# Optimization experiments

Hardware: AMD Instinct MI355X
Metric: run time of the kernel (lower is better)

## Reference

```python
import jax, jax.numpy as jnp
import numpy as np

N, F_NODE, F_FLOW, H, E, B, L = 131072, 64, 16, 128, 2097152, 256, 32


def setup_inputs() -> dict:
    key = jax.random.key(0)
    ks = jax.random.split(key, 24)
    gn = lambda k, s, sc: jax.random.normal(k, s, jnp.float32) * sc
    s_in = 1.0 / np.sqrt(F_NODE)
    s_h = 1.0 / np.sqrt(H)
    s_f = 1.0 / np.sqrt(F_FLOW)
    s_c = 1.0 / np.sqrt(2 * H + H // 2)
    inp = {
        "x": gn(ks[0], (N, F_NODE), 1.0),
        "edge_index": jax.random.randint(ks[1], (2, E), 0, N),
        "batch": jnp.sort(jax.random.randint(ks[2], (N,), 0, B)),
        "path_idx": jax.random.randint(ks[3], (B, L), 0, N),
        "path_len": jax.random.randint(ks[4], (B,), 1, L + 1),
        "flow": gn(ks[5], (B, F_FLOW), 1.0),
        # SAGEConv1: out = mean_agg(x_j) @ Wl.T + b + x_i @ Wr.T
        "Wl1": gn(ks[6], (H, F_NODE), s_in), "Wr1": gn(ks[7], (H, F_NODE), s_in), "b1": gn(ks[8], (H,), s_in),
        "Wl2": gn(ks[9], (H, H), s_h), "Wr2": gn(ks[10], (H, H), s_h), "b2": gn(ks[11], (H,), s_h),
        # LSTM (torch gate order i,f,g,o)
        "Wih": gn(ks[12], (4 * H, H), s_h), "Whh": gn(ks[13], (4 * H, H), s_h),
        "bih": gn(ks[14], (4 * H,), s_h), "bhh": gn(ks[15], (4 * H,), s_h),
        # flow encoder Linear(F_FLOW, H//2)
        "Wf": gn(ks[16], (H // 2, F_FLOW), s_f), "bf": gn(ks[17], (H // 2,), s_f),
        # scorer MLP: Linear(2H+H//2, H) -> ReLU -> Linear(H, 1)
        "Ws1": gn(ks[18], (H, 2 * H + H // 2), s_c), "bs1": gn(ks[19], (H,), s_c),
        "Ws2": gn(ks[20], (1, H), s_h), "bs2": gn(ks[21], (1,), s_h),
    }
    return inp


def _sage(x, src, dst, Wl, Wr, b, n):
    agg = jax.ops.segment_sum(x[src], dst, num_segments=n)  # [n, d]
    cnt = jax.ops.segment_sum(jnp.ones((src.shape[0],), x.dtype), dst, num_segments=n)
    mean = agg / jnp.maximum(cnt, 1.0)[:, None]
    return mean @ Wl.T + b + x @ Wr.T


def _lstm_final_h(seq, valid, Wih, Whh, bih, bhh):
    # seq: [B, L, H], valid: [B, L] bool; returns h at each path's last valid step
    b, l, h = seq.shape
    h0 = jnp.zeros((b, h), seq.dtype)

    def step(carry, inp):
        hp, cp = carry
        x_t, v = inp  # [B,H], [B]
        gates = x_t @ Wih.T + hp @ Whh.T + bih + bhh
        i, f, g, o = jnp.split(gates, 4, axis=-1)
        c_new = jax.nn.sigmoid(f) * cp + jax.nn.sigmoid(i) * jnp.tanh(g)
        h_new = jax.nn.sigmoid(o) * jnp.tanh(c_new)
        m = v[:, None]
        return (jnp.where(m, h_new, hp), jnp.where(m, c_new, cp)), None

    (hf, _), _ = jax.lax.scan(step, (h0, h0),
                              (jnp.swapaxes(seq, 0, 1), jnp.swapaxes(valid, 0, 1)))
    return hf


def reference(x, edge_index, batch, path_idx, path_len, flow,
              Wl1, Wr1, b1, Wl2, Wr2, b2,
              Wih, Whh, bih, bhh, Wf, bf, Ws1, bs1, Ws2, bs2):
    n = x.shape[0]
    src, dst = edge_index[0], edge_index[1]
    h1 = jax.nn.relu(_sage(x, src, dst, Wl1, Wr1, b1, n))
    node_emb = jax.nn.relu(_sage(h1, src, dst, Wl2, Wr2, b2, n))

    # global mean pool per graph
    gsum = jax.ops.segment_sum(node_emb, batch, num_segments=B)
    gcnt = jax.ops.segment_sum(jnp.ones((n,), node_emb.dtype), batch, num_segments=B)
    graph_emb = gsum / jnp.maximum(gcnt, 1.0)[:, None]  # [B, H]

    flow_emb = jax.nn.relu(flow @ Wf.T + bf)  # [B, H//2]

    path_seq = node_emb[path_idx]  # [B, L, H]
    valid = jnp.arange(L)[None, :] < path_len[:, None]  # [B, L]
    path_emb = _lstm_final_h(path_seq, valid, Wih, Whh, bih, bhh)  # [B, H]

    combined = jnp.concatenate([graph_emb, path_emb, flow_emb], axis=-1)
    hidden = jax.nn.relu(combined @ Ws1.T + bs1)
    scores = hidden @ Ws2.T + bs2  # [B, 1]
    return scores[:, 0]  # matches torch.cat of per-path [1] outputs -> [B]
```

## Files before the change

kernel.cpp:

```cpp
#include <hip/hip_runtime.h>
#include <hip/hip_bf16.h>

#define N_NODES 131072
#define N_EDGES 2097152
#define BATCHES 256
#define LPATH   32
#define NB   256
#define NPB  512
#define GB   256
#define EPB  8192

typedef __hip_bfloat16 bf16;
using short8  = __attribute__((ext_vector_type(8))) short;
using floatx4 = __attribute__((ext_vector_type(4))) float;
using floatx2 = __attribute__((ext_vector_type(2))) float;

__device__ __forceinline__ float bl(unsigned u){ union {unsigned x; float f;} c; c.x = u << 16; return c.f; }
__device__ __forceinline__ float bh(unsigned u){ union {unsigned x; float f;} c; c.x = u & 0xffff0000u; return c.f; }
__device__ __forceinline__ unsigned packbf(float lo, float hi){
  bf16 l = __float2bfloat16(lo), h = __float2bfloat16(hi);
  unsigned short lu, hu;
  __builtin_memcpy(&lu, &l, 2); __builtin_memcpy(&hu, &h, 2);
  return (unsigned)lu | ((unsigned)hu << 16);
}
__device__ __forceinline__ float frcp(float x){ return __builtin_amdgcn_rcpf(x); }
__device__ __forceinline__ float sigf(float x){ return frcp(1.f + __expf(-x)); }
__device__ __forceinline__ float tanh_fast(float x){ return fmaf(2.f, frcp(1.f + __expf(-2.f * x)), -1.f); }

__global__ void prep_k(const float* __restrict__ Wl1, const float* __restrict__ Wr1,
                       const float* __restrict__ Wl2, const float* __restrict__ Wr2,
                       const float* __restrict__ Wih, const float* __restrict__ Whh,
                       const float* __restrict__ bih, const float* __restrict__ bhh,
                       bf16* __restrict__ Wcat1, bf16* __restrict__ Wcat2,
                       bf16* __restrict__ WihB, bf16* __restrict__ WhhB, float* __restrict__ bsumF){
  int g = blockIdx.x * 256 + threadIdx.x;
  if (g < 16384) {
    int h = g >> 7, k = g & 127;
    float v = (k < 64) ? Wl1[h * 64 + k] : Wr1[h * 64 + (k - 64)];
    Wcat1[g] = __float2bfloat16(v);
  } else if (g < 49152) {
    int q = g - 16384;
    int h = q >> 8, k = q & 255;
    float v = (k < 128) ? Wl2[h * 128 + k] : Wr2[h * 128 + (k - 128)];
    Wcat2[q] = __float2bfloat16(v);
  } else if (g < 114688) {
    int q = g - 49152;
    WihB[q] = __float2bfloat16(Wih[q]);
  } else if (g < 180224) {
    int q = g - 114688;
    WhhB[q] = __float2bfloat16(Whh[q]);
  } else if (g < 180736) {
    int k = g - 180224;
    bsumF[k] = bih[k] + bhh[k];
  }
}

__global__ void xb8_k(const float* __restrict__ x, unsigned* __restrict__ xb8, bf16* __restrict__ Acat1){
  int g = blockIdx.x * 256 + threadIdx.x;
  int n = g >> 4, p = g & 15;
  float4 v = *(const float4*)(x + (size_t)n * 64 + p * 4);
  uint2 wb; wb.x = packbf(v.x, v.y); wb.y = packbf(v.z, v.w);
  *(uint2*)(Acat1 + (size_t)n * 128 + 64 + p * 4) = wb;
  int w = 0;
  w = __builtin_amdgcn_cvt_pk_fp8_f32(v.x, v.y, w, false);
  w = __builtin_amdgcn_cvt_pk_fp8_f32(v.z, v.w, w, true);
  xb8[(size_t)n * 16 + p] = (unsigned)w;
}

__global__ void bounds_k(const int* __restrict__ batch, int* __restrict__ starts){
  int b = threadIdx.x;
  int lo = 0, hi = N_NODES;
  while (lo < hi){ int mid = (lo + hi) >> 1; if (batch[mid] < b) lo = mid + 1; else hi = mid; }
  starts[b] = lo;
  if (b == 0) starts[BATCHES] = N_NODES;
}

__global__ void cntA_k(const int* __restrict__ dst, int* __restrict__ cntA){
  __shared__ int h[NB];
  int tid = threadIdx.x;
  h[tid] = 0;
  __syncthreads();
  int base = blockIdx.x * EPB;
  #pragma unroll
  for (int i = 0; i < EPB / 256; ++i){
    int d = dst[base + i * 256 + tid];
    atomicAdd(&h[d >> 9], 1);
  }
  __syncthreads();
  cntA[tid * GB + blockIdx.x] = h[tid];
}

__global__ void scan1_k(const int* __restrict__ cnt, int* __restrict__ ofsA, int* __restrict__ bsum){
  __shared__ int sh[256];
  int t = threadIdx.x, i = blockIdx.x * 256 + t;
  int v = cnt[i];
  sh[t] = v; __syncthreads();
  int inc = v;
  for (int d = 1; d < 256; d <<= 1){
    int add = (t >= d) ? sh[t - d] : 0;
    __syncthreads();
    inc += add; sh[t] = inc;
    __syncthreads();
  }
  ofsA[i] = inc - v;
  if (t == 255) bsum[blockIdx.x] = inc;
}

__global__ void scan2_k(const int* __restrict__ bsum, int* __restrict__ bsumEx){
  __shared__ int sh[NB];
  int t = threadIdx.x;
  int v = bsum[t];
  sh[t] = v; __syncthreads();
  int inc = v;
  for (int d = 1; d < NB; d <<= 1){
    int add = (t >= d) ? sh[t - d] : 0;
    __syncthreads();
    inc += add; sh[t] = inc;
    __syncthreads();
  }
  bsumEx[t] = inc - v;
}

__global__ void passA2_k(const int* __restrict__ src, const int* __restrict__ dst,
                         const int* __restrict__ ofsA, const int* __restrict__ bsumEx,
                         unsigned* __restrict__ ebuf){
  __shared__ int cur[NB];
  int tid = threadIdx.x;
  cur[tid] = ofsA[tid * GB + blockIdx.x] + bsumEx[tid];
  __syncthreads();
  int base = blockIdx.x * EPB;
  #pragma unroll
  for (int i = 0; i < EPB / 256; ++i){
    int e = base + i * 256 + tid;
    int s = src[e], d = dst[e];
    int p = atomicAdd(&cur[d >> 9], 1);
    ebuf[p] = (unsigned)s | ((unsigned)(d & (NPB - 1)) << 17);
  }
}

__global__ void passB_k(const unsigned* __restrict__ ebuf, const int* __restrict__ bsumEx,
                        int* __restrict__ offs, int* __restrict__ srcS){
  __shared__ int ncnt[NPB];
  __shared__ int pairs[256];
  __shared__ int nofs[NPB];
  int k = blockIdx.x, tid = threadIdx.x;
  int bs = bsumEx[k];
  int be = (k < NB - 1) ? bsumEx[k + 1] : N_EDGES;
  ncnt[tid] = 0; ncnt[tid + 256] = 0;
  __syncthreads();
  for (int i = bs + tid; i < be; i += 256)
    atomicAdd(&ncnt[ebuf[i] >> 17], 1);
  __syncthreads();
  int p = ncnt[2 * tid] + ncnt[2 * tid + 1];
  pairs[tid] = p;
  __syncthreads();
  int inc = p;
  for (int d = 1; d < 256; d <<= 1){
    int add = (tid >= d) ? pairs[tid - d] : 0;
    __syncthreads();
    inc += add; pairs[tid] = inc;
    __syncthreads();
  }
  int ex = inc - p;
  nofs[2 * tid]     = ex;
  nofs[2 * tid + 1] = ex + ncnt[2 * tid];
  __syncthreads();
  offs[k * NPB + tid]       = bs + nofs[tid];
  offs[k * NPB + tid + 256] = bs + nofs[tid + 256];
  if (k == NB - 1 && tid == 0) offs[N_NODES] = N_EDGES;
  ncnt[tid] = nofs[tid]; ncnt[tid + 256] = nofs[tid + 256];
  __syncthreads();
  for (int i = bs + tid; i < be; i += 256){
    unsigned w = ebuf[i];
    int loc = w >> 17, sv = w & 0x1FFFF;
    int pp = atomicAdd(&ncnt[loc], 1);
    srcS[bs + pp] = sv;
  }
}

__global__ void agg1_k(const unsigned* __restrict__ xb8, const int* __restrict__ offs,
                       const int* __restrict__ srcS, bf16* __restrict__ Acat1){
  int wid = threadIdx.x >> 6, lane = threadIdx.x & 63;
  int n = blockIdx.x * 4 + wid;
  int s = offs[n], e = offs[n + 1];
  int slot = lane >> 3, fl = lane & 7;
  floatx2 a0={0,0}, a1={0,0}, a2={0,0}, a3={0,0};
  floatx2 c0={0,0}, c1={0,0}, c2={0,0}, c3={0,0};
  int i = s + slot;
  for (; i + 8 < e; i += 16){
    int sv0 = srcS[i], sv1 = srcS[i + 8];
    uint2 u = *(const uint2*)(xb8 + (size_t)sv0 * 16 + fl * 2);
    uint2 v = *(const uint2*)(xb8 + (size_t)sv1 * 16 + fl * 2);
    a0 += __builtin_amdgcn_cvt_pk_f32_fp8(u.x, false);
    a1 += __builtin_amdgcn_cvt_pk_f32_fp8(u.x, true);
    a2 += __builtin_amdgcn_cvt_pk_f32_fp8(u.y, false);
    a3 += __builtin_amdgcn_cvt_pk_f32_fp8(u.y, true);
    c0 += __builtin_amdgcn_cvt_pk_f32_fp8(v.x, false);
    c1 += __builtin_amdgcn_cvt_pk_f32_fp8(v.x, true);
    c2 += __builtin_amdgcn_cvt_pk_f32_fp8(v.y, false);
    c3 += __builtin_amdgcn_cvt_pk_f32_fp8(v.y, true);
  }
  if (i < e){
    int sv0 = srcS[i];
    uint2 u = *(const uint2*)(xb8 + (size_t)sv0 * 16 + fl * 2);
    a0 += __builtin_amdgcn_cvt_pk_f32_fp8(u.x, false);
    a1 += __builtin_amdgcn_cvt_pk_f32_fp8(u.x, true);
    a2 += __builtin_amdgcn_cvt_pk_f32_fp8(u.y, false);
    a3 += __builtin_amdgcn_cvt_pk_f32_fp8(u.y, true);
  }
  a0 += c0; a1 += c1; a2 += c2; a3 += c3;
  float f[8] = {a0.x, a0.y, a1.x, a1.y, a2.x, a2.y, a3.x, a3.y};
  #pragma unroll
  for (int j = 0; j < 8; ++j){
    f[j] += __shfl_xor(f[j], 8);
    f[j] += __shfl_xor(f[j], 16);
    f[j] += __shfl_xor(f[j], 32);
  }
  if (slot == 0){
    int d = e - s; if (d < 1) d = 1;
    float inv = 1.f / (float)d;
    uint4 w;
    w.x = packbf(f[0] * inv, f[1] * inv);
    w.y = packbf(f[2] * inv, f[3] * inv);
    w.z = packbf(f[4] * inv, f[5] * inv);
    w.w = packbf(f[6] * inv, f[7] * inv);
    *(uint4*)(Acat1 + (size_t)n * 128 + fl * 8) = w;
  }
}

__global__ void cvt8_k(const bf16* __restrict__ Acat2, unsigned* __restrict__ h1f8){
  int g = blockIdx.x * 256 + threadIdx.x;
  int n = g >> 5, p = g & 31;
  uint2 u = *(const uint2*)(Acat2 + (size_t)n * 256 + 128 + p * 4);
  int w = 0;
  w = __builtin_amdgcn_cvt_pk_fp8_f32(bl(u.x), bh(u.x), w, false);
  w = __builtin_amdgcn_cvt_pk_fp8_f32(bl(u.y), bh(u.y), w, true);
  h1f8[(size_t)n * 32 + p] = (unsigned)w;
}

__global__ void agg2_k(const int* __restrict__ offs, const int* __restrict__ srcS,
                       const unsigned* __restrict__ h1f8, bf16* __restrict__ Acat2){
  int wid = threadIdx.x >> 6, lane = threadIdx.x & 63;
  int n = blockIdx.x * 4 + wid;
  int s = offs[n], e = offs[n + 1];
  int slot = lane >> 4, fl = lane & 15;
  floatx2 a0={0,0}, a1={0,0}, a2={0,0}, a3={0,0};
  floatx2 c0={0,0}, c1={0,0}, c2={0,0}, c3={0,0};
  int i = s + slot;
  for (; i + 4 < e; i += 8){
    int sv0 = srcS[i], sv1 = srcS[i + 4];
    uint2 u = *(const uint2*)(h1f8 + (size_t)sv0 * 32 + fl * 2);
    uint2 v = *(const uint2*)(h1f8 + (size_t)sv1 * 32 + fl * 2);
    a0 += __builtin_amdgcn_cvt_pk_f32_fp8(u.x, false);
    a1 += __builtin_amdgcn_cvt_pk_f32_fp8(u.x, true);
    a2 += __builtin_amdgcn_cvt_pk_f32_fp8(u.y, false);
    a3 += __builtin_amdgcn_cvt_pk_f32_fp8(u.y, true);
    c0 += __builtin_amdgcn_cvt_pk_f32_fp8(v.x, false);
    c1 += __builtin_amdgcn_cvt_pk_f32_fp8(v.x, true);
    c2 += __builtin_amdgcn_cvt_pk_f32_fp8(v.y, false);
    c3 += __builtin_amdgcn_cvt_pk_f32_fp8(v.y, true);
  }
  if (i < e){
    int sv0 = srcS[i];
    uint2 u = *(const uint2*)(h1f8 + (size_t)sv0 * 32 + fl * 2);
    a0 += __builtin_amdgcn_cvt_pk_f32_fp8(u.x, false);
    a1 += __builtin_amdgcn_cvt_pk_f32_fp8(u.x, true);
    a2 += __builtin_amdgcn_cvt_pk_f32_fp8(u.y, false);
    a3 += __builtin_amdgcn_cvt_pk_f32_fp8(u.y, true);
  }
  a0 += c0; a1 += c1; a2 += c2; a3 += c3;
  float f[8] = {a0.x, a0.y, a1.x, a1.y, a2.x, a2.y, a3.x, a3.y};
  #pragma unroll
  for (int j = 0; j < 8; ++j){
    f[j] += __shfl_xor(f[j], 16);
    f[j] += __shfl_xor(f[j], 32);
  }
  if (slot == 0){
    int d = e - s; if (d < 1) d = 1;
    float inv = 1.f / (float)d;
    uint4 w;
    w.x = packbf(f[0] * inv, f[1] * inv);
    w.y = packbf(f[2] * inv, f[3] * inv);
    w.z = packbf(f[4] * inv, f[5] * inv);
    w.w = packbf(f[6] * inv, f[7] * inv);
    *(uint4*)(Acat2 + (size_t)n * 256 + fl * 8) = w;
  }
}

__global__ __launch_bounds__(256) void gemm_k(const bf16* __restrict__ A, int lda,
                                              const bf16* __restrict__ W, int K,
                                              const float* __restrict__ bias,
                                              void* __restrict__ out, int ldo, int outF32, int relu,
                                              const int* __restrict__ ridx){
  __shared__ bf16 Wl[128][136];
  int tid = threadIdx.x;
  int wid = tid >> 6, lane = tid & 63;
  int l16 = lane & 15, quad = lane >> 4;
  int rowBase  = blockIdx.x * 64 + wid * 16;
  int colGroup = blockIdx.y * 128;
  int arow = rowBase + l16;
  if (ridx) arow = ridx[arow];
  floatx4 acc[8] = {};
  int nStage = K >> 7;
  for (int ks = 0; ks < nStage; ++ks){
    __syncthreads();
    for (int c = tid; c < 2048; c += 256){
      int r = c >> 4, kc = (c & 15) << 3;
      *(uint4*)(&Wl[r][kc]) = *(const uint4*)(W + (size_t)(colGroup + r) * K + ks * 128 + kc);
    }
    __syncthreads();
    for (int kk = 0; kk < 4; ++kk){
      short8 af = *(const short8*)(A + (size_t)arow * lda + ks * 128 + kk * 32 + quad * 8);
      #pragma unroll
      for (int c = 0; c < 8; ++c){
        short8 bq = *(const short8*)(&Wl[c * 16 + l16][kk * 32 + quad * 8]);
        acc[c] = __builtin_amdgcn_mfma_f32_16x16x32_bf16(af, bq, acc[c], 0, 0, 0);
      }
    }
  }
  #pragma unroll
  for (int c = 0; c < 8; ++c){
    int col = colGroup + c * 16 + l16;
    float bv = bias ? bias[col] : 0.f;
    #pragma unroll
    for (int r = 0; r < 4; ++r){
      int row = rowBase + quad * 4 + r;
      float v = acc[c][r] + bv;
      if (relu) v = fmaxf(v, 0.f);
      if (outF32) ((float*)out)[(size_t)row * ldo + col] = v;
      else        ((bf16*)out)[(size_t)row * ldo + col]  = __float2bfloat16(v);
    }
  }
}

__global__ void pool_k(const bf16* __restrict__ ne, const int* __restrict__ starts, float* __restrict__ comb){
  __shared__ float sh[8][128];
  int b = blockIdx.x;
  int q = threadIdx.x >> 6, lane = threadIdx.x & 63;
  int s = starts[b], e = starts[b + 1];
  float a0 = 0.f, a1 = 0.f;
  for (int i = s + q; i < e; i += 8){
    unsigned u = *(const unsigned*)(ne + (size_t)i * 128 + lane * 2);
    a0 += bl(u); a1 += bh(u);
  }
  sh[q][lane * 2] = a0; sh[q][lane * 2 + 1] = a1;
  __syncthreads();
  if (threadIdx.x < 128){
    int f = threadIdx.x;
    float tot = 0.f;
    #pragma unroll
    for (int k = 0; k < 8; ++k) tot += sh[k][f];
    int d = e - s; if (d < 1) d = 1;
    comb[b * 320 + f] = tot / (float)d;
  }
}

__global__ void flow_k(const float* __restrict__ flow, const float* __restrict__ Wf,
                       const float* __restrict__ bfv, float* __restrict__ comb){
  int g = blockIdx.x * 256 + threadIdx.x;
  int b = g >> 6, j = g & 63;
  float acc = bfv[j];
  for (int k = 0; k < 16; ++k)
    acc += flow[b * 16 + k] * Wf[j * 16 + k];
  comb[b * 320 + 256 + j] = fmaxf(acc, 0.f);
}

__global__ __launch_bounds__(256, 1) void lstm_k(const bf16* __restrict__ Whh, const float* __restrict__ pre,
                                                 const int* __restrict__ path_len, float* __restrict__ comb){
  __shared__ bf16 hbuf[2][16][136];
  int tid = threadIdx.x;
  int w = tid >> 6, lane = tid & 63;
  int l16 = lane & 15, quad = lane >> 4;
  int b0 = blockIdx.x * 16;

  short8 wb[4][2][4];
  #pragma unroll
  for (int q = 0; q < 4; ++q)
    #pragma unroll
    for (int hf = 0; hf < 2; ++hf){
      const bf16* rp = Whh + (size_t)(q * 128 + w * 32 + hf * 16 + l16) * 128 + quad * 8;
      #pragma unroll
      for (int ks = 0; ks < 4; ++ks) wb[q][hf][ks] = *(const short8*)(rp + ks * 32);
    }

  int lenr[4];
  #pragma unroll
  for (int r = 0; r < 4; ++r){
    int L = path_len[b0 + quad * 4 + r];
    if (L < 1) L = 1; if (L > LPATH) L = LPATH;
    lenr[r] = L;
  }
  int maxlen = 1;
  for (int i = 0; i < 16; ++i){
    int L = path_len[b0 + i];
    if (L > LPATH) L = LPATH;
    if (L > maxlen) maxlen = L;
  }

  for (int i = tid; i < 1088; i += 256) ((unsigned*)&hbuf[0][0][0])[i] = 0;

  const float* pb[4];
  #pragma unroll
  for (int r = 0; r < 4; ++r)
    pb[r] = pre + (size_t)(b0 + quad * 4 + r) * LPATH * 512 + w * 32 + l16;

  float pv[4][2][4];
  #pragma unroll
  for (int q = 0; q < 4; ++q)
    #pragma unroll
    for (int hf = 0; hf < 2; ++hf)
      #pragma unroll
      for (int r = 0; r < 4; ++r)
        pv[q][hf][r] = pb[r][q * 128 + hf * 16];

  float cst[2][4] = {}, hst[2][4] = {};

  for (int t = 0; t < maxlen; ++t){
    int cur = t & 1, nxt = cur ^ 1;
    __syncthreads();
    short8 af[4];
    #pragma unroll
    for (int ks = 0; ks < 4; ++ks)
      af[ks] = *(const short8*)(&hbuf[cur][l16][ks * 32 + quad * 8]);
    int tn = (t + 1 < maxlen) ? t + 1 : t;
    float pnext[4][2][4];
    #pragma unroll
    for (int q = 0; q < 4; ++q)
      #pragma unroll
      for (int hf = 0; hf < 2; ++hf)
        #pragma unroll
        for (int r = 0; r < 4; ++r)
          pnext[q][hf][r] = pb[r][tn * 512 + q * 128 + hf * 16];
    floatx4 acc[4][2];
    #pragma unroll
    for (int q = 0; q < 4; ++q)
      #pragma unroll
      for (int hf = 0; hf < 2; ++hf){
        acc[q][hf][0] = pv[q][hf][0]; acc[q][hf][1] = pv[q][hf][1];
        acc[q][hf][2] = pv[q][hf][2]; acc[q][hf][3] = pv[q][hf][3];
      }
    #pragma unroll
    for (int ks = 0; ks < 4; ++ks)
      #pragma unroll
      for (int q = 0; q < 4; ++q)
        #pragma unroll
        for (int hf = 0; hf < 2; ++hf)
          acc[q][hf] = __builtin_amdgcn_mfma_f32_16x16x32_bf16(af[ks], wb[q][hf][ks], acc[q][hf], 0, 0, 0);
    #pragma unroll
    for (int hf = 0; hf < 2; ++hf)
      #pragma unroll
      for (int r = 0; r < 4; ++r){
        float ig = sigf(acc[0][hf][r]);
        float fg = sigf(acc[1][hf][r]);
        float gg = tanh_fast(acc[2][hf][r]);
        float og = sigf(acc[3][hf][r]);
        float cn = fmaf(fg, cst[hf][r], ig * gg);
        float hn = og * tanh_fast(cn);
        bool vld = t < lenr[r];
        cst[hf][r] = vld ? cn : cst[hf][r];
        hst[hf][r] = vld ? hn : hst[hf][r];
        hbuf[nxt][quad * 4 + r][w * 32 + hf * 16 + l16] = __float2bfloat16(hst[hf][r]);
      }
    #pragma unroll
    for (int q = 0; q < 4; ++q)
      #pragma unroll
      for (int hf = 0; hf < 2; ++hf)
        #pragma unroll
        for (int r = 0; r < 4; ++r)
          pv[q][hf][r] = pnext[q][hf][r];
  }

  #pragma unroll
  for (int hf = 0; hf < 2; ++hf)
    #pragma unroll
    for (int r = 0; r < 4; ++r)
      comb[(b0 + quad * 4 + r) * 320 + 128 + w * 32 + hf * 16 + l16] = hst[hf][r];
}

__global__ void head_k(const float* __restrict__ comb, const float* __restrict__ Ws1, const float* __restrict__ bs1,
                       const float* __restrict__ Ws2, const float* __restrict__ bs2, float* __restrict__ out){
  __shared__ float cl[320];
  __shared__ float red[128];
  int b = blockIdx.x, j = threadIdx.x;
  for (int k = j; k < 320; k += 128) cl[k] = comb[b * 320 + k];
  __syncthreads();
  float acc = bs1[j];
  const float4* wr = (const float4*)(Ws1 + (size_t)j * 320);
  #pragma unroll 4
  for (int kc = 0; kc < 80; ++kc){
    float4 u = wr[kc];
    int k = kc * 4;
    acc += u.x * cl[k] + u.y * cl[k + 1] + u.z * cl[k + 2] + u.w * cl[k + 3];
  }
  float hv = fmaxf(acc, 0.f);
  red[j] = hv * Ws2[j];
  __syncthreads();
  for (int s = 64; s > 0; s >>= 1){ if (j < s) red[j] += red[j + s]; __syncthreads(); }
  if (j == 0) out[b] = red[0] + bs2[0];
}

constexpr size_t OFF_OFFS   = 0;
constexpr size_t OFF_CNTA   = 524544;
constexpr size_t OFF_OFSA   = OFF_CNTA   + 262144;
constexpr size_t OFF_BSUM   = OFF_OFSA   + 262144;
constexpr size_t OFF_BSUMEX = OFF_BSUM   + 1024;
constexpr size_t OFF_STARTS = OFF_BSUMEX + 1024;
constexpr size_t OFF_SRCS   = OFF_STARTS + 2048;
constexpr size_t OFF_WCAT1  = OFF_SRCS   + 8388608;
constexpr size_t OFF_WCAT2  = OFF_WCAT1  + 32768;
constexpr size_t OFF_WIHB   = OFF_WCAT2  + 65536;
constexpr size_t OFF_WHHB   = OFF_WIHB   + 131072;
constexpr size_t OFF_BSUMF  = OFF_WHHB   + 131072;
constexpr size_t OFF_COMB   = OFF_BSUMF  + 2048;
constexpr size_t OFF_ACAT1  = OFF_COMB   + 327680;
constexpr size_t OFF_ACAT2  = OFF_ACAT1  + 33554432;
constexpr size_t OFF_H1F8   = OFF_ACAT1;
constexpr size_t OFF_EBUF   = OFF_ACAT2;
constexpr size_t OFF_PRE    = OFF_ACAT2  + 2097152;
constexpr size_t OFF_XB8    = OFF_ACAT2  + 50331648;

extern "C" void kernel_launch(void* const* d_in, const int* in_sizes, int n_in,
                              void* d_out, int out_size, void* d_ws, size_t ws_size,
                              hipStream_t stream){
  const float* x      = (const float*)d_in[0];
  const int* edge     = (const int*)d_in[1];
  const int* batch    = (const int*)d_in[2];
  const int* path_idx = (const int*)d_in[3];
  const int* path_len = (const int*)d_in[4];
  const float* flow   = (const float*)d_in[5];
  const float* Wl1 = (const float*)d_in[6];
  const float* Wr1 = (const float*)d_in[7];
  const float* b1  = (const float*)d_in[8];
  const float* Wl2 = (const float*)d_in[9];
  const float* Wr2 = (const float*)d_in[10];
  const float* b2  = (const float*)d_in[11];
  const float* Wih = (const float*)d_in[12];
  const float* Whh = (const float*)d_in[13];
  const float* bih = (const float*)d_in[14];
  const float* bhh = (const float*)d_in[15];
  const float* Wf  = (const float*)d_in[16];
  const float* bfv = (const float*)d_in[17];
  const float* Ws1 = (const float*)d_in[18];
  const float* bs1 = (const float*)d_in[19];
  const float* Ws2 = (const float*)d_in[20];
  const float* bs2 = (const float*)d_in[21];

  char* ws = (char*)d_ws;
  int* offs    = (int*)(ws + OFF_OFFS);
  int* cntA    = (int*)(ws + OFF_CNTA);
  int* ofsA    = (int*)(ws + OFF_OFSA);
  int* bsum    = (int*)(ws + OFF_BSUM);
  int* bsumEx  = (int*)(ws + OFF_BSUMEX);
  int* starts  = (int*)(ws + OFF_STARTS);
  int* srcS    = (int*)(ws + OFF_SRCS);
  bf16* Wcat1  = (bf16*)(ws + OFF_WCAT1);
  bf16* Wcat2  = (bf16*)(ws + OFF_WCAT2);
  bf16* WihB   = (bf16*)(ws + OFF_WIHB);
  bf16* WhhB   = (bf16*)(ws + OFF_WHHB);
  float* bsumF = (float*)(ws + OFF_BSUMF);
  float* comb  = (float*)(ws + OFF_COMB);
  bf16* Acat1  = (bf16*)(ws + OFF_ACAT1);
  bf16* node_emb = Acat1;
  bf16* Acat2  = (bf16*)(ws + OFF_ACAT2);
  unsigned* h1f8 = (unsigned*)(ws + OFF_H1F8);
  unsigned* ebuf = (unsigned*)(ws + OFF_EBUF);
  float* pre   = (float*)(ws + OFF_PRE);
  unsigned* xb8 = (unsigned*)(ws + OFF_XB8);

  prep_k<<<707, 256, 0, stream>>>(Wl1, Wr1, Wl2, Wr2, Wih, Whh, bih, bhh, Wcat1, Wcat2, WihB, WhhB, bsumF);
  xb8_k<<<N_NODES / 16, 256, 0, stream>>>(x, xb8, Acat1);
  bounds_k<<<1, 256, 0, stream>>>(batch, starts);
  cntA_k<<<GB, 256, 0, stream>>>(edge + N_EDGES, cntA);
  scan1_k<<<NB, 256, 0, stream>>>(cntA, ofsA, bsum);
  scan2_k<<<1, NB, 0, stream>>>(bsum, bsumEx);
  passA2_k<<<GB, 256, 0, stream>>>(edge, edge + N_EDGES, ofsA, bsumEx, ebuf);
  passB_k<<<NB, 256, 0, stream>>>(ebuf, bsumEx, offs, srcS);
  agg1_k<<<N_NODES / 4, 256, 0, stream>>>(xb8, offs, srcS, Acat1);
  gemm_k<<<dim3(N_NODES / 64, 1), 256, 0, stream>>>(Acat1, 128, Wcat1, 128, b1, Acat2 + 128, 256, 0, 1, nullptr);
  cvt8_k<<<N_NODES / 8, 256, 0, stream>>>(Acat2, h1f8);
  agg2_k<<<N_NODES / 4, 256, 0, stream>>>(offs, srcS, h1f8, Acat2);
  gemm_k<<<dim3(N_NODES / 64, 1), 256, 0, stream>>>(Acat2, 256, Wcat2, 256, b2, node_emb, 128, 0, 1, nullptr);
  pool_k<<<BATCHES, 512, 0, stream>>>(node_emb, starts, comb);
  flow_k<<<64, 256, 0, stream>>>(flow, Wf, bfv, comb);
  gemm_k<<<dim3(BATCHES * LPATH / 64, 4), 256, 0, stream>>>(node_emb, 128, WihB, 128, bsumF, pre, 512, 1, 0, path_idx);
  lstm_k<<<BATCHES / 16, 256, 0, stream>>>(WhhB, pre, path_len, comb);
  head_k<<<BATCHES, 128, 0, stream>>>(comb, Ws1, bs1, Ws2, bs2, (float*)d_out);
}
```

Baseline: 444.6 us.

## Merge small prep kernels into fused launches and unroll agg2 gather loop

```diff
diff --git a/kernel.cpp b/kernel.cpp
--- a/kernel.cpp
+++ b/kernel.cpp
@@ -27,67 +27,67 @@
 __device__ __forceinline__ float sigf(float x){ return frcp(1.f + __expf(-x)); }
 __device__ __forceinline__ float tanh_fast(float x){ return fmaf(2.f, frcp(1.f + __expf(-2.f * x)), -1.f); }
 
-__global__ void prep_k(const float* __restrict__ Wl1, const float* __restrict__ Wr1,
-                       const float* __restrict__ Wl2, const float* __restrict__ Wr2,
-                       const float* __restrict__ Wih, const float* __restrict__ Whh,
-                       const float* __restrict__ bih, const float* __restrict__ bhh,
-                       bf16* __restrict__ Wcat1, bf16* __restrict__ Wcat2,
-                       bf16* __restrict__ WihB, bf16* __restrict__ WhhB, float* __restrict__ bsumF){
-  int g = blockIdx.x * 256 + threadIdx.x;
-  if (g < 16384) {
-    int h = g >> 7, k = g & 127;
-    float v = (k < 64) ? Wl1[h * 64 + k] : Wr1[h * 64 + (k - 64)];
-    Wcat1[g] = __float2bfloat16(v);
-  } else if (g < 49152) {
-    int q = g - 16384;
-    int h = q >> 8, k = q & 255;
-    float v = (k < 128) ? Wl2[h * 128 + k] : Wr2[h * 128 + (k - 128)];
-    Wcat2[q] = __float2bfloat16(v);
-  } else if (g < 114688) {
-    int q = g - 49152;
-    WihB[q] = __float2bfloat16(Wih[q]);
-  } else if (g < 180224) {
-    int q = g - 114688;
-    WhhB[q] = __float2bfloat16(Whh[q]);
-  } else if (g < 180736) {
-    int k = g - 180224;
-    bsumF[k] = bih[k] + bhh[k];
-  }
-}
-
-__global__ void xb8_k(const float* __restrict__ x, unsigned* __restrict__ xb8, bf16* __restrict__ Acat1){
-  int g = blockIdx.x * 256 + threadIdx.x;
-  int n = g >> 4, p = g & 15;
-  float4 v = *(const float4*)(x + (size_t)n * 64 + p * 4);
-  uint2 wb; wb.x = packbf(v.x, v.y); wb.y = packbf(v.z, v.w);
-  *(uint2*)(Acat1 + (size_t)n * 128 + 64 + p * 4) = wb;
-  int w = 0;
-  w = __builtin_amdgcn_cvt_pk_fp8_f32(v.x, v.y, w, false);
-  w = __builtin_amdgcn_cvt_pk_fp8_f32(v.z, v.w, w, true);
-  xb8[(size_t)n * 16 + p] = (unsigned)w;
-}
-
-__global__ void bounds_k(const int* __restrict__ batch, int* __restrict__ starts){
-  int b = threadIdx.x;
-  int lo = 0, hi = N_NODES;
-  while (lo < hi){ int mid = (lo + hi) >> 1; if (batch[mid] < b) lo = mid + 1; else hi = mid; }
-  starts[b] = lo;
-  if (b == 0) starts[BATCHES] = N_NODES;
-}
-
-__global__ void cntA_k(const int* __restrict__ dst, int* __restrict__ cntA){
+__global__ void mega0_k(const float* __restrict__ x, unsigned* __restrict__ xb8, bf16* __restrict__ Acat1,
+                        const int* __restrict__ dst, int* __restrict__ cntA,
+                        const float* __restrict__ Wl1, const float* __restrict__ Wr1,
+                        const float* __restrict__ Wl2, const float* __restrict__ Wr2,
+                        const float* __restrict__ Wih, const float* __restrict__ Whh,
+                        const float* __restrict__ bih, const float* __restrict__ bhh,
+                        bf16* __restrict__ Wcat1, bf16* __restrict__ Wcat2,
+                        bf16* __restrict__ WihB, bf16* __restrict__ WhhB, float* __restrict__ bsumF,
+                        const int* __restrict__ batch, int* __restrict__ starts){
   __shared__ int h[NB];
-  int tid = threadIdx.x;
-  h[tid] = 0;
-  __syncthreads();
-  int base = blockIdx.x * EPB;
-  #pragma unroll
-  for (int i = 0; i < EPB / 256; ++i){
-    int d = dst[base + i * 256 + tid];
-    atomicAdd(&h[d >> 9], 1);
-  }
-  __syncthreads();
-  cntA[tid * GB + blockIdx.x] = h[tid];
+  int bid = blockIdx.x, tid = threadIdx.x;
+  if (bid < 8192){
+    int g = bid * 256 + tid;
+    int n = g >> 4, p = g & 15;
+    float4 v = *(const float4*)(x + (size_t)n * 64 + p * 4);
+    uint2 wb; wb.x = packbf(v.x, v.y); wb.y = packbf(v.z, v.w);
+    *(uint2*)(Acat1 + (size_t)n * 128 + 64 + p * 4) = wb;
+    int w = 0;
+    w = __builtin_amdgcn_cvt_pk_fp8_f32(v.x, v.y, w, false);
+    w = __builtin_amdgcn_cvt_pk_fp8_f32(v.z, v.w, w, true);
+    xb8[(size_t)n * 16 + p] = (unsigned)w;
+  } else if (bid < 8448){
+    int cb = bid - 8192;
+    h[tid] = 0;
+    __syncthreads();
+    int base = cb * EPB;
+    #pragma unroll
+    for (int i = 0; i < EPB / 256; ++i){
+      int d = dst[base + i * 256 + tid];
+      atomicAdd(&h[d >> 9], 1);
+    }
+    __syncthreads();
+    cntA[tid * GB + cb] = h[tid];
+  } else if (bid < 9155){
+    int g = (bid - 8448) * 256 + tid;
+    if (g < 16384) {
+      int hh = g >> 7, k = g & 127;
+      float v = (k < 64) ? Wl1[hh * 64 + k] : Wr1[hh * 64 + (k - 64)];
+      Wcat1[g] = __float2bfloat16(v);
+    } else if (g < 49152) {
+      int q = g - 16384;
+      int hh = q >> 8, k = q & 255;
+      float v = (k < 128) ? Wl2[hh * 128 + k] : Wr2[hh * 128 + (k - 128)];
+      Wcat2[q] = __float2bfloat16(v);
+    } else if (g < 114688) {
+      int q = g - 49152;
+      WihB[q] = __float2bfloat16(Wih[q]);
+    } else if (g < 180224) {
+      int q = g - 114688;
+      WhhB[q] = __float2bfloat16(Whh[q]);
+    } else if (g < 180736) {
+      int k = g - 180224;
+      bsumF[k] = bih[k] + bhh[k];
+    }
+  } else {
+    int b = tid;
+    int lo = 0, hi = N_NODES;
+    while (lo < hi){ int mid = (lo + hi) >> 1; if (batch[mid] < b) lo = mid + 1; else hi = mid; }
+    starts[b] = lo;
+    if (b == 0) starts[BATCHES] = N_NODES;
+  }
 }
 
 __global__ void scan1_k(const int* __restrict__ cnt, int* __restrict__ ofsA, int* __restrict__ bsum){
@@ -106,27 +106,22 @@
   if (t == 255) bsum[blockIdx.x] = inc;
 }
 
-__global__ void scan2_k(const int* __restrict__ bsum, int* __restrict__ bsumEx){
-  __shared__ int sh[NB];
-  int t = threadIdx.x;
-  int v = bsum[t];
-  sh[t] = v; __syncthreads();
+__global__ void passA2_k(const int* __restrict__ src, const int* __restrict__ dst,
+                         const int* __restrict__ ofsA, const int* __restrict__ bsum,
+                         unsigned* __restrict__ ebuf){
+  __shared__ int cur[NB];
+  __shared__ int sc[NB];
+  int tid = threadIdx.x;
+  int v = bsum[tid];
+  sc[tid] = v; __syncthreads();
   int inc = v;
   for (int d = 1; d < NB; d <<= 1){
-    int add = (t >= d) ? sh[t - d] : 0;
-    __syncthreads();
-    inc += add; sh[t] = inc;
-    __syncthreads();
-  }
-  bsumEx[t] = inc - v;
-}
-
-__global__ void passA2_k(const int* __restrict__ src, const int* __restrict__ dst,
-                         const int* __restrict__ ofsA, const int* __restrict__ bsumEx,
-                         unsigned* __restrict__ ebuf){
-  __shared__ int cur[NB];
-  int tid = threadIdx.x;
-  cur[tid] = ofsA[tid * GB + blockIdx.x] + bsumEx[tid];
+    int add = (tid >= d) ? sc[tid - d] : 0;
+    __syncthreads();
+    inc += add; sc[tid] = inc;
+    __syncthreads();
+  }
+  cur[tid] = ofsA[tid * GB + blockIdx.x] + (inc - v);
   __syncthreads();
   int base = blockIdx.x * EPB;
   #pragma unroll
@@ -138,14 +133,26 @@
   }
 }
 
-__global__ void passB_k(const unsigned* __restrict__ ebuf, const int* __restrict__ bsumEx,
+__global__ void passB_k(const unsigned* __restrict__ ebuf, const int* __restrict__ bsum,
                         int* __restrict__ offs, int* __restrict__ srcS){
   __shared__ int ncnt[NPB];
   __shared__ int pairs[256];
   __shared__ int nofs[NPB];
+  __shared__ int sc[NB];
   int k = blockIdx.x, tid = threadIdx.x;
-  int bs = bsumEx[k];
-  int be = (k < NB - 1) ? bsumEx[k + 1] : N_EDGES;
+  int v = bsum[tid];
+  sc[tid] = v; __syncthreads();
+  int inc0 = v;
+  for (int d = 1; d < NB; d <<= 1){
+    int add = (tid >= d) ? sc[tid - d] : 0;
+    __syncthreads();
+    inc0 += add; sc[tid] = inc0;
+    __syncthreads();
+  }
+  sc[tid] = inc0 - v;
+  __syncthreads();
+  int bs = sc[k];
+  int be = (k < NB - 1) ? sc[k + 1] : N_EDGES;
   ncnt[tid] = 0; ncnt[tid + 256] = 0;
   __syncthreads();
   for (int i = bs + tid; i < be; i += 256)
@@ -245,22 +252,34 @@
   int s = offs[n], e = offs[n + 1];
   int slot = lane >> 4, fl = lane & 15;
   floatx2 a0={0,0}, a1={0,0}, a2={0,0}, a3={0,0};
+  floatx2 b0={0,0}, b1={0,0}, b2={0,0}, b3={0,0};
   floatx2 c0={0,0}, c1={0,0}, c2={0,0}, c3={0,0};
+  floatx2 d0={0,0}, d1={0,0}, d2={0,0}, d3={0,0};
   int i = s + slot;
-  for (; i + 4 < e; i += 8){
-    int sv0 = srcS[i], sv1 = srcS[i + 4];
+  for (; i + 12 < e; i += 16){
+    int sv0 = srcS[i], sv1 = srcS[i + 4], sv2 = srcS[i + 8], sv3 = srcS[i + 12];
     uint2 u = *(const uint2*)(h1f8 + (size_t)sv0 * 32 + fl * 2);
     uint2 v = *(const uint2*)(h1f8 + (size_t)sv1 * 32 + fl * 2);
+    uint2 w = *(const uint2*)(h1f8 + (size_t)sv2 * 32 + fl * 2);
+    uint2 z = *(const uint2*)(h1f8 + (size_t)sv3 * 32 + fl * 2);
     a0 += __builtin_amdgcn_cvt_pk_f32_fp8(u.x, false);
     a1 += __builtin_amdgcn_cvt_pk_f32_fp8(u.x, true);
     a2 += __builtin_amdgcn_cvt_pk_f32_fp8(u.y, false);
     a3 += __builtin_amdgcn_cvt_pk_f32_fp8(u.y, true);
-    c0 += __builtin_amdgcn_cvt_pk_f32_fp8(v.x, false);
-    c1 += __builtin_amdgcn_cvt_pk_f32_fp8(v.x, true);
-    c2 += __builtin_amdgcn_cvt_pk_f32_fp8(v.y, false);
-    c3 += __builtin_amdgcn_cvt_pk_f32_fp8(v.y, true);
-  }
-  if (i < e){
+    b0 += __builtin_amdgcn_cvt_pk_f32_fp8(v.x, false);
+    b1 += __builtin_amdgcn_cvt_pk_f32_fp8(v.x, true);
+    b2 += __builtin_amdgcn_cvt_pk_f32_fp8(v.y, false);
+    b3 += __builtin_amdgcn_cvt_pk_f32_fp8(v.y, true);
+    c0 += __builtin_amdgcn_cvt_pk_f32_fp8(w.x, false);
+    c1 += __builtin_amdgcn_cvt_pk_f32_fp8(w.x, true);
+    c2 += __builtin_amdgcn_cvt_pk_f32_fp8(w.y, false);
+    c3 += __builtin_amdgcn_cvt_pk_f32_fp8(w.y, true);
+    d0 += __builtin_amdgcn_cvt_pk_f32_fp8(z.x, false);
+    d1 += __builtin_amdgcn_cvt_pk_f32_fp8(z.x, true);
+    d2 += __builtin_amdgcn_cvt_pk_f32_fp8(z.y, false);
+    d3 += __builtin_amdgcn_cvt_pk_f32_fp8(z.y, true);
+  }
+  for (; i < e; i += 4){
     int sv0 = srcS[i];
     uint2 u = *(const uint2*)(h1f8 + (size_t)sv0 * 32 + fl * 2);
     a0 += __builtin_amdgcn_cvt_pk_f32_fp8(u.x, false);
@@ -268,6 +287,8 @@
     a2 += __builtin_amdgcn_cvt_pk_f32_fp8(u.y, false);
     a3 += __builtin_amdgcn_cvt_pk_f32_fp8(u.y, true);
   }
+  a0 += b0; a1 += b1; a2 += b2; a3 += b3;
+  c0 += d0; c1 += d1; c2 += d2; c3 += d3;
   a0 += c0; a1 += c1; a2 += c2; a3 += c3;
   float f[8] = {a0.x, a0.y, a1.x, a1.y, a2.x, a2.y, a3.x, a3.y};
   #pragma unroll
@@ -333,36 +354,38 @@
   }
 }
 
-__global__ void pool_k(const bf16* __restrict__ ne, const int* __restrict__ starts, float* __restrict__ comb){
+__global__ void poolflow_k(const bf16* __restrict__ ne, const int* __restrict__ starts,
+                           const float* __restrict__ flow, const float* __restrict__ Wf,
+                           const float* __restrict__ bfv, float* __restrict__ comb){
   __shared__ float sh[8][128];
-  int b = blockIdx.x;
-  int q = threadIdx.x >> 6, lane = threadIdx.x & 63;
-  int s = starts[b], e = starts[b + 1];
-  float a0 = 0.f, a1 = 0.f;
-  for (int i = s + q; i < e; i += 8){
-    unsigned u = *(const unsigned*)(ne + (size_t)i * 128 + lane * 2);
-    a0 += bl(u); a1 += bh(u);
-  }
-  sh[q][lane * 2] = a0; sh[q][lane * 2 + 1] = a1;
-  __syncthreads();
-  if (threadIdx.x < 128){
-    int f = threadIdx.x;
-    float tot = 0.f;
-    #pragma unroll
-    for (int k = 0; k < 8; ++k) tot += sh[k][f];
-    int d = e - s; if (d < 1) d = 1;
-    comb[b * 320 + f] = tot / (float)d;
-  }
-}
-
-__global__ void flow_k(const float* __restrict__ flow, const float* __restrict__ Wf,
-                       const float* __restrict__ bfv, float* __restrict__ comb){
-  int g = blockIdx.x * 256 + threadIdx.x;
-  int b = g >> 6, j = g & 63;
-  float acc = bfv[j];
-  for (int k = 0; k < 16; ++k)
-    acc += flow[b * 16 + k] * Wf[j * 16 + k];
-  comb[b * 320 + 256 + j] = fmaxf(acc, 0.f);
+  int bid = blockIdx.x;
+  if (bid < 256){
+    int b = bid;
+    int q = threadIdx.x >> 6, lane = threadIdx.x & 63;
+    int s = starts[b], e = starts[b + 1];
+    float a0 = 0.f, a1 = 0.f;
+    for (int i = s + q; i < e; i += 8){
+      unsigned u = *(const unsigned*)(ne + (size_t)i * 128 + lane * 2);
+      a0 += bl(u); a1 += bh(u);
+    }
+    sh[q][lane * 2] = a0; sh[q][lane * 2 + 1] = a1;
+    __syncthreads();
+    if (threadIdx.x < 128){
+      int f = threadIdx.x;
+      float tot = 0.f;
+      #pragma unroll
+      for (int k = 0; k < 8; ++k) tot += sh[k][f];
+      int d = e - s; if (d < 1) d = 1;
+      comb[b * 320 + f] = tot / (float)d;
+    }
+  } else {
+    int g = (bid - 256) * 512 + threadIdx.x;
+    int b = g >> 6, j = g & 63;
+    float acc = bfv[j];
+    for (int k = 0; k < 16; ++k)
+      acc += flow[b * 16 + k] * Wf[j * 16 + k];
+    comb[b * 320 + 256 + j] = fmaxf(acc, 0.f);
+  }
 }
 
 __global__ __launch_bounds__(256, 1) void lstm_k(const bf16* __restrict__ Whh, const float* __restrict__ pre,
@@ -503,8 +526,7 @@
 constexpr size_t OFF_CNTA   = 524544;
 constexpr size_t OFF_OFSA   = OFF_CNTA   + 262144;
 constexpr size_t OFF_BSUM   = OFF_OFSA   + 262144;
-constexpr size_t OFF_BSUMEX = OFF_BSUM   + 1024;
-constexpr size_t OFF_STARTS = OFF_BSUMEX + 1024;
+constexpr size_t OFF_STARTS = OFF_BSUM   + 1024;
 constexpr size_t OFF_SRCS   = OFF_STARTS + 2048;
 constexpr size_t OFF_WCAT1  = OFF_SRCS   + 8388608;
 constexpr size_t OFF_WCAT2  = OFF_WCAT1  + 32768;
@@ -550,7 +572,6 @@
   int* cntA    = (int*)(ws + OFF_CNTA);
   int* ofsA    = (int*)(ws + OFF_OFSA);
   int* bsum    = (int*)(ws + OFF_BSUM);
-  int* bsumEx  = (int*)(ws + OFF_BSUMEX);
   int* starts  = (int*)(ws + OFF_STARTS);
   int* srcS    = (int*)(ws + OFF_SRCS);
   bf16* Wcat1  = (bf16*)(ws + OFF_WCAT1);
@@ -567,21 +588,18 @@
   float* pre   = (float*)(ws + OFF_PRE);
   unsigned* xb8 = (unsigned*)(ws + OFF_XB8);
 
-  prep_k<<<707, 256, 0, stream>>>(Wl1, Wr1, Wl2, Wr2, Wih, Whh, bih, bhh, Wcat1, Wcat2, WihB, WhhB, bsumF);
-  xb8_k<<<N_NODES / 16, 256, 0, stream>>>(x, xb8, Acat1);
-  bounds_k<<<1, 256, 0, stream>>>(batch, starts);
-  cntA_k<<<GB, 256, 0, stream>>>(edge + N_EDGES, cntA);
+  mega0_k<<<9156, 256, 0, stream>>>(x, xb8, Acat1, edge + N_EDGES, cntA,
+                                    Wl1, Wr1, Wl2, Wr2, Wih, Whh, bih, bhh,
+                                    Wcat1, Wcat2, WihB, WhhB, bsumF, batch, starts);
   scan1_k<<<NB, 256, 0, stream>>>(cntA, ofsA, bsum);
-  scan2_k<<<1, NB, 0, stream>>>(bsum, bsumEx);
-  passA2_k<<<GB, 256, 0, stream>>>(edge, edge + N_EDGES, ofsA, bsumEx, ebuf);
-  passB_k<<<NB, 256, 0, stream>>>(ebuf, bsumEx, offs, srcS);
+  passA2_k<<<GB, 256, 0, stream>>>(edge, edge + N_EDGES, ofsA, bsum, ebuf);
+  passB_k<<<NB, 256, 0, stream>>>(ebuf, bsum, offs, srcS);
   agg1_k<<<N_NODES / 4, 256, 0, stream>>>(xb8, offs, srcS, Acat1);
   gemm_k<<<dim3(N_NODES / 64, 1), 256, 0, stream>>>(Acat1, 128, Wcat1, 128, b1, Acat2 + 128, 256, 0, 1, nullptr);
   cvt8_k<<<N_NODES / 8, 256, 0, stream>>>(Acat2, h1f8);
   agg2_k<<<N_NODES / 4, 256, 0, stream>>>(offs, srcS, h1f8, Acat2);
   gemm_k<<<dim3(N_NODES / 64, 1), 256, 0, stream>>>(Acat2, 256, Wcat2, 256, b2, node_emb, 128, 0, 1, nullptr);
-  pool_k<<<BATCHES, 512, 0, stream>>>(node_emb, starts, comb);
-  flow_k<<<64, 256, 0, stream>>>(flow, Wf, bfv, comb);
+  poolflow_k<<<288, 512, 0, stream>>>(node_emb, starts, flow, Wf, bfv, comb);
   gemm_k<<<dim3(BATCHES * LPATH / 64, 4), 256, 0, stream>>>(node_emb, 128, WihB, 128, bsumF, pre, 512, 1, 0, path_idx);
   lstm_k<<<BATCHES / 16, 256, 0, stream>>>(WhhB, pre, path_len, comb);
   head_k<<<BATCHES, 128, 0, stream>>>(comb, Ws1, bs1, Ws2, bs2, (float*)d_out);
```

Result: no change. 438.7 us (-1.3%).
